# Kernel optimization log

Hardware: AMD Instinct MI355X
Metric: run time of the kernel (lower is better)

## Reference

```python
import jax, jax.numpy as jnp
import numpy as np

D_MODEL = 192
D_STATE = 16
D_CONV = 4
EXPAND = 2
D_INNER = EXPAND * D_MODEL          # 384
DT_RANK = (D_MODEL + 15) // 16       # 12
B_, C_, DD, HH, WW = 2, 192, 32, 32, 16


def setup_inputs() -> dict:
    key = jax.random.key(0)
    ks = jax.random.split(key, 10)
    s = 0.02
    return {
        "x": jax.random.normal(ks[0], (B_, C_, DD, HH, WW), jnp.float32),
        # Mamba params (mamba-ssm layout)
        "in_proj_w": jax.random.normal(ks[1], (2 * D_INNER, D_MODEL), jnp.float32) * s,
        "conv_w": jax.random.normal(ks[2], (D_INNER, 1, D_CONV), jnp.float32) * s,
        "conv_b": jnp.zeros((D_INNER,), jnp.float32),
        "x_proj_w": jax.random.normal(ks[3], (DT_RANK + 2 * D_STATE, D_INNER), jnp.float32) * s,
        "dt_proj_w": jax.random.normal(ks[4], (D_INNER, DT_RANK), jnp.float32) * s,
        # bias chosen so softplus(dt) is small/positive, as in mamba's dt init
        "dt_proj_b": jax.random.uniform(ks[5], (D_INNER,), jnp.float32, minval=-4.0, maxval=-2.0),
        "A_log": jnp.log(jnp.broadcast_to(jnp.arange(1, D_STATE + 1, dtype=jnp.float32), (D_INNER, D_STATE))),
        "D_param": jnp.ones((D_INNER,), jnp.float32),
        "out_proj_w": jax.random.normal(ks[6], (D_MODEL, D_INNER), jnp.float32) * s,
        # 1x1x1 Conv3d projection (input_dim -> output_dim)
        "proj_w": jax.random.normal(ks[7], (C_, C_), jnp.float32) * s,
        "proj_b": jnp.zeros((C_,), jnp.float32),
    }


def _mamba(xf, in_proj_w, conv_w, conv_b, x_proj_w, dt_proj_w, dt_proj_b, A_log, D_param, out_proj_w):
    # xf: (B, L, d_model)
    B, L, _ = xf.shape
    xz = xf @ in_proj_w.T                          # (B, L, 2*d_inner)
    u, z = jnp.split(xz, 2, axis=-1)               # each (B, L, d_inner)

    # causal depthwise conv1d over L, kernel D_CONV
    uc = jnp.transpose(u, (0, 2, 1))               # (B, d_inner, L)
    up = jnp.pad(uc, ((0, 0), (0, 0), (D_CONV - 1, 0)))
    conv = sum(up[:, :, k:k + L] * conv_w[None, :, 0, k, None] for k in range(D_CONV))
    conv = conv + conv_b[None, :, None]
    u = jax.nn.silu(jnp.transpose(conv, (0, 2, 1)))  # (B, L, d_inner)

    dbl = u @ x_proj_w.T                           # (B, L, dt_rank + 2*d_state)
    dt_low = dbl[..., :DT_RANK]
    Bm = dbl[..., DT_RANK:DT_RANK + D_STATE]       # (B, L, d_state)
    Cm = dbl[..., DT_RANK + D_STATE:]              # (B, L, d_state)
    dt = jax.nn.softplus(dt_low @ dt_proj_w.T + dt_proj_b)  # (B, L, d_inner)

    A = -jnp.exp(A_log)                            # (d_inner, d_state)

    def step(h, inputs):
        u_t, dt_t, B_t, C_t = inputs               # (B,d_inner),(B,d_inner),(B,d_state),(B,d_state)
        dA = jnp.exp(dt_t[..., None] * A)          # (B, d_inner, d_state)
        h = dA * h + dt_t[..., None] * B_t[:, None, :] * u_t[..., None]
        y = jnp.einsum('bds,bs->bd', h, C_t)
        return h, y

    h0 = jnp.zeros((B, D_INNER, D_STATE), xf.dtype)
    xs = (jnp.transpose(u, (1, 0, 2)), jnp.transpose(dt, (1, 0, 2)),
          jnp.transpose(Bm, (1, 0, 2)), jnp.transpose(Cm, (1, 0, 2)))
    _, ys = jax.lax.scan(step, h0, xs)             # ys: (L, B, d_inner)
    y = jnp.transpose(ys, (1, 0, 2)) + u * D_param
    y = y * jax.nn.silu(z)
    return y @ out_proj_w.T                        # (B, L, d_model)


def reference(x, in_proj_w, conv_w, conv_b, x_proj_w, dt_proj_w, dt_proj_b,
              A_log, D_param, out_proj_w, proj_w, proj_b):
    B, C, Dz, H, W = x.shape
    # InstanceNorm3d (affine=False, eps=1e-5, biased variance)
    mu = x.mean(axis=(2, 3, 4), keepdims=True)
    var = x.var(axis=(2, 3, 4), keepdims=True)
    xn = (x - mu) / jnp.sqrt(var + 1e-5)
    L = Dz * H * W
    xf = jnp.transpose(xn.reshape(B, C, L), (0, 2, 1))  # (B, L, C)
    y = _mamba(xf, in_proj_w, conv_w, conv_b, x_proj_w, dt_proj_w, dt_proj_b,
               A_log, D_param, out_proj_w)
    y = jnp.transpose(y, (0, 2, 1)).reshape(B, C, Dz, H, W)
    # 1x1x1 Conv3d projection
    out = jnp.einsum('bcdhw,oc->bodhw', y, proj_w) + proj_b[None, :, None, None, None]
    return out
```

## Files before the change

### kernel.cpp

```cpp
#include <hip/hip_runtime.h>
#include <hip/hip_bf16.h>
#include <hip/hip_fp16.h>
#include <math.h>

#define BB   2
#define CM   192
#define DI   384
#define LL   16384
#define NST  16
#define RDT  12
#define XJ   44
#define NC   512
#define CLEN 32
#define NCH  (NC / 16)
#define DBS  64
#define XZS  768
#define CVT  32
#define BK   32

typedef __attribute__((ext_vector_type(8))) short bf16x8;
typedef __attribute__((ext_vector_type(4))) float f32x4;
typedef __attribute__((ext_vector_type(2))) float f32x2;
typedef unsigned short ushort_t;

static __device__ __forceinline__ ushort_t f2bf(float f) {
  __hip_bfloat16 h = __float2bfloat16(f);
  return *reinterpret_cast<ushort_t*>(&h);
}
static __device__ __forceinline__ float bf2f(ushort_t u) {
  __hip_bfloat16 h;
  *reinterpret_cast<ushort_t*>(&h) = u;
  return __bfloat162float(h);
}
static __device__ __forceinline__ ushort_t f2h(float f) {
  __half h = __float2half(f);
  return *reinterpret_cast<ushort_t*>(&h);
}
static __device__ __forceinline__ float h2f(ushort_t u) {
  __half h;
  *reinterpret_cast<ushort_t*>(&h) = u;
  return __half2float(h);
}

__global__ __launch_bounds__(256) void fuse_proj_kernel(
    const float* __restrict__ pw, const float* __restrict__ ow, float* __restrict__ PW) {
  int idx = blockIdx.x * 256 + threadIdx.x;
  if (idx >= CM * DI) return;
  int o = idx / DI, d = idx % DI;
  float s = 0.f;
  #pragma unroll 4
  for (int c = 0; c < CM; c++) s += pw[o * CM + c] * ow[c * DI + d];
  PW[idx] = s;
}

__global__ __launch_bounds__(256) void cvt_weights_kernel(
    const float* __restrict__ ipw, const float* __restrict__ xpw,
    const float* __restrict__ PW,
    ushort_t* __restrict__ ipw_bf, ushort_t* __restrict__ xpw_bf,
    ushort_t* __restrict__ PW_bf) {
  int i = blockIdx.x * 256 + threadIdx.x;
  if (i < 2 * DI * CM) ipw_bf[i] = f2bf(ipw[i]);
  if (i < 128 * DI) {
    int r = i / DI;
    xpw_bf[i] = (r < XJ) ? f2bf(xpw[i]) : (ushort_t)0;
  }
  if (i < 256 * DI) {
    int r = i / DI;
    PW_bf[i] = (r < CM) ? f2bf(PW[i]) : (ushort_t)0;
  }
}

__global__ __launch_bounds__(256) void norm_stats_kernel(
    const float* __restrict__ x, float* __restrict__ mu, float* __restrict__ rstd) {
  int bc = blockIdx.x;
  const float* p = x + (size_t)bc * LL;
  float s = 0.f, ss = 0.f;
  for (int i = threadIdx.x * 4; i < LL; i += 256 * 4) {
    float4 v = *(const float4*)(p + i);
    s += v.x + v.y + v.z + v.w;
    ss += v.x * v.x + v.y * v.y + v.z * v.z + v.w * v.w;
  }
  for (int o = 32; o > 0; o >>= 1) {
    s += __shfl_down(s, o, 64);
    ss += __shfl_down(ss, o, 64);
  }
  __shared__ float sb[4], ssb[4];
  int wid = threadIdx.x >> 6;
  if ((threadIdx.x & 63) == 0) { sb[wid] = s; ssb[wid] = ss; }
  __syncthreads();
  if (threadIdx.x == 0) {
    s = sb[0] + sb[1] + sb[2] + sb[3];
    ss = ssb[0] + ssb[1] + ssb[2] + ssb[3];
    float m = s * (1.f / LL);
    float var = ss * (1.f / LL) - m * m;
    mu[bc] = m;
    rstd[bc] = 1.f / sqrtf(var + 1e-5f);
  }
}

__global__ __launch_bounds__(256) void xt_norm_kernel(
    const float* __restrict__ x, const float* __restrict__ mu,
    const float* __restrict__ rstd, ushort_t* __restrict__ xT) {
  __shared__ ushort_t T[64][72];
  int t0 = blockIdx.x * 64, c0 = blockIdx.y * 64, b = blockIdx.z;
  int tid = threadIdx.x;
  int c = tid >> 2, tq = (tid & 3) * 16;
  int bc = b * CM + c0 + c;
  const float* xp = x + (size_t)bc * LL + t0 + tq;
  float m = mu[bc], rs = rstd[bc];
  #pragma unroll
  for (int j = 0; j < 16; j += 4) {
    float4 v = *(const float4*)(xp + j);
    T[c][tq + j + 0] = f2bf((v.x - m) * rs);
    T[c][tq + j + 1] = f2bf((v.y - m) * rs);
    T[c][tq + j + 2] = f2bf((v.z - m) * rs);
    T[c][tq + j + 3] = f2bf((v.w - m) * rs);
  }
  __syncthreads();
  int t = tid >> 2, cq = (tid & 3) * 16;
  unsigned int ob[8];
  #pragma unroll
  for (int j = 0; j < 8; j++)
    ob[j] = (unsigned int)T[cq + 2 * j][t] | ((unsigned int)T[cq + 2 * j + 1][t] << 16);
  ushort_t* op = xT + ((size_t)b * LL + t0 + t) * CM + c0 + cq;
  *(uint4*)(op)     = make_uint4(ob[0], ob[1], ob[2], ob[3]);
  *(uint4*)(op + 8) = make_uint4(ob[4], ob[5], ob[6], ob[7]);
}

template <bool TOUT, typename OutT>
__global__ __launch_bounds__(256) void gemm_lds(
    const ushort_t* __restrict__ A, const ushort_t* __restrict__ BT,
    OutT* __restrict__ C, int K, int Mreal, int MT,
    long strideBT, long strideC, int ldc,
    const float* __restrict__ bias) {
  __shared__ ushort_t Asm[2][128 * BK];
  __shared__ ushort_t Bsm[2][128 * BK];

  int id = blockIdx.x;
  int per = MT * 8;
  int g = id / per, r = id % per;
  int nt = g * 8 + (r & 7);
  int mt = r >> 3;
  int b  = nt >> 7;
  long n0 = (long)(nt & 127) * 128;
  int m0 = mt * 128;

  int tid = threadIdx.x;
  int lane = tid & 63, wave = tid >> 6;
  const ushort_t* Bbase = BT + (size_t)b * strideBT;

  int srow0 = wave * 32 + (lane >> 2);
  int sk = (lane & 3) * 8;

  f32x4 acc[4][4];
  #pragma unroll
  for (int mi = 0; mi < 4; mi++)
    #pragma unroll
    for (int ni = 0; ni < 4; ni++) acc[mi][ni] = (f32x4){0.f, 0.f, 0.f, 0.f};

  int mh = wave & 1, nh = wave >> 1;
  int fr = lane & 15, fk = (lane >> 4) * 8;

  int nsteps = K / BK;
  {
    const ushort_t* As0 = A + (size_t)(m0 + srow0) * K + sk;
    const ushort_t* Bs0 = Bbase + (size_t)(n0 + srow0) * K + sk;
    __builtin_amdgcn_global_load_lds(As0, &Asm[0][wave * 1024], 16, 0, 0);
    __builtin_amdgcn_global_load_lds(As0 + (size_t)16 * K, &Asm[0][wave * 1024 + 512], 16, 0, 0);
    __builtin_amdgcn_global_load_lds(Bs0, &Bsm[0][wave * 1024], 16, 0, 0);
    __builtin_amdgcn_global_load_lds(Bs0 + (size_t)16 * K, &Bsm[0][wave * 1024 + 512], 16, 0, 0);
  }
  __syncthreads();
  int cur = 0;
  for (int s = 0; s < nsteps; s++) {
    if (s + 1 < nsteps) {
      int k0 = (s + 1) * BK;
      const ushort_t* As0 = A + (size_t)(m0 + srow0) * K + k0 + sk;
      const ushort_t* Bs0 = Bbase + (size_t)(n0 + srow0) * K + k0 + sk;
      __builtin_amdgcn_global_load_lds(As0, &Asm[cur ^ 1][wave * 1024], 16, 0, 0);
      __builtin_amdgcn_global_load_lds(As0 + (size_t)16 * K, &Asm[cur ^ 1][wave * 1024 + 512], 16, 0, 0);
      __builtin_amdgcn_global_load_lds(Bs0, &Bsm[cur ^ 1][wave * 1024], 16, 0, 0);
      __builtin_amdgcn_global_load_lds(Bs0 + (size_t)16 * K, &Bsm[cur ^ 1][wave * 1024 + 512], 16, 0, 0);
    }
    bf16x8 fa[4], fb[4];
    #pragma unroll
    for (int mi = 0; mi < 4; mi++)
      fa[mi] = *(const bf16x8*)&Asm[cur][(mh * 64 + mi * 16 + fr) * BK + fk];
    #pragma unroll
    for (int ni = 0; ni < 4; ni++)
      fb[ni] = *(const bf16x8*)&Bsm[cur][(nh * 64 + ni * 16 + fr) * BK + fk];
    #pragma unroll
    for (int mi = 0; mi < 4; mi++)
      #pragma unroll
      for (int ni = 0; ni < 4; ni++) {
        if constexpr (TOUT)
          acc[mi][ni] = __builtin_amdgcn_mfma_f32_16x16x32_bf16(fb[ni], fa[mi], acc[mi][ni], 0, 0, 0);
        else
          acc[mi][ni] = __builtin_amdgcn_mfma_f32_16x16x32_bf16(fa[mi], fb[ni], acc[mi][ni], 0, 0, 0);
      }
    __syncthreads();
    cur ^= 1;
  }

  int cq = (lane >> 4) * 4;
  if constexpr (TOUT) {
    #pragma unroll
    for (int ni = 0; ni < 4; ni++)
      #pragma unroll
      for (int rg = 0; rg < 4; rg++) {
        long n = n0 + nh * 64 + ni * 16 + cq + rg;
        OutT* cp = C + (size_t)b * strideC + n * ldc + m0 + mh * 64 + fr;
        #pragma unroll
        for (int mi = 0; mi < 4; mi++) {
          int mrow = m0 + mh * 64 + mi * 16 + fr;
          if (mrow < Mreal) {
            float v = acc[mi][ni][rg];
            if constexpr (sizeof(OutT) == 2) cp[mi * 16] = f2bf(v);
            else                             cp[mi * 16] = v;
          }
        }
      }
  } else {
    #pragma unroll
    for (int mi = 0; mi < 4; mi++)
      #pragma unroll
      for (int rg = 0; rg < 4; rg++) {
        int m = m0 + mh * 64 + mi * 16 + cq + rg;
        if (m < Mreal) {
          float bv = bias ? bias[m] : 0.f;
          OutT* cp = C + (size_t)b * strideC + (size_t)m * ldc + n0 + nh * 64 + fr;
          #pragma unroll
          for (int ni = 0; ni < 4; ni++)
            cp[ni * 16] = acc[mi][ni][rg] + bv;
        }
      }
  }
}

__global__ __launch_bounds__(384) void conv_silu_kernel(
    const ushort_t* __restrict__ xzT, const float* __restrict__ conv_w,
    const float* __restrict__ conv_b, ushort_t* __restrict__ u_t) {
  __shared__ ushort_t Us[CVT + 3][DI];
  int t0 = blockIdx.x * CVT;
  int b = blockIdx.y;
  int tid = threadIdx.x;
  #pragma unroll
  for (int r = 0; r < CVT + 3; r++) {
    int t = t0 - 3 + r;
    Us[r][tid] = (t >= 0) ? xzT[((size_t)b * LL + t) * XZS + tid] : (ushort_t)0;
  }
  float w0 = conv_w[tid * 4 + 0], w1 = conv_w[tid * 4 + 1];
  float w2 = conv_w[tid * 4 + 2], w3 = conv_w[tid * 4 + 3];
  float cb = conv_b[tid];
  __syncthreads();
  ushort_t* up = u_t + ((size_t)b * LL + t0) * DI + tid;
  float xm3 = bf2f(Us[0][tid]);
  float xm2 = bf2f(Us[1][tid]);
  float xm1 = bf2f(Us[2][tid]);
  #pragma unroll
  for (int t = 0; t < CVT; t++) {
    float xc = bf2f(Us[t + 3][tid]);
    float a = cb + w3 * xc + w2 * xm1 + w1 * xm2 + w0 * xm3;
    float sv = a / (1.f + __expf(-a));
    up[(size_t)t * DI] = f2bf(sv);
    xm3 = xm2; xm2 = xm1; xm1 = xc;
  }
}

__global__ __launch_bounds__(128) void scan_phase1(
    const ushort_t* __restrict__ u_t, const float* __restrict__ dblT,
    const float* __restrict__ A_log,
    const float* __restrict__ dtw, const float* __restrict__ dtb,
    float* __restrict__ hend, float* __restrict__ Sbuf,
    ushort_t* __restrict__ dt16) {
  int chunk = blockIdx.x, b = blockIdx.z;
  int d = blockIdx.y * 128 + threadIdx.x;
  int t0 = chunk * CLEN;
  const float* dblB = dblT + ((size_t)b * LL + t0) * DBS;
  int bd = b * DI + d;
  float av0 = -expf(A_log[d * NST]);
  float av_[NST];
  bool ok = true;
  #pragma unroll
  for (int j = 0; j < NST; j++) {
    av_[j] = -expf(A_log[d * NST + j]);
    ok = ok && (fabsf(av_[j] - av0 * (float)(j + 1)) <= 1e-4f * fabsf(av_[j]));
  }
  float w12[12];
  #pragma unroll
  for (int rr = 0; rr < 12; rr += 4)
    *(float4*)(w12 + rr) = *(const float4*)(dtw + d * 12 + rr);
  float db = dtb[d];
  const ushort_t* up = u_t + ((size_t)b * LL + t0) * DI + d;
  ushort_t* dtp16 = dt16 + ((size_t)b * LL + t0) * DI + d;
  float S = 0.f;

  size_t o = ((size_t)bd * NC + chunk) * NST;
  if (__all(ok)) {
    f32x2 h2[8];
    #pragma unroll
    for (int j = 0; j < 8; j++) h2[j] = (f32x2){0.f, 0.f};
    #pragma unroll 4
    for (int t = 0; t < CLEN; t++) {
      float4 L0 = *(const float4*)(dblB + t * DBS + 0);
      float4 L1 = *(const float4*)(dblB + t * DBS + 4);
      float4 L2 = *(const float4*)(dblB + t * DBS + 8);
      float4 B0 = *(const float4*)(dblB + t * DBS + RDT + 0);
      float4 B1 = *(const float4*)(dblB + t * DBS + RDT + 4);
      float4 B2 = *(const float4*)(dblB + t * DBS + RDT + 8);
      float4 B3 = *(const float4*)(dblB + t * DBS + RDT + 12);
      float acc = db;
      acc = fmaf(L0.x, w12[0], acc); acc = fmaf(L0.y, w12[1], acc);
      acc = fmaf(L0.z, w12[2], acc); acc = fmaf(L0.w, w12[3], acc);
      acc = fmaf(L1.x, w12[4], acc); acc = fmaf(L1.y, w12[5], acc);
      acc = fmaf(L1.z, w12[6], acc); acc = fmaf(L1.w, w12[7], acc);
      acc = fmaf(L2.x, w12[8], acc); acc = fmaf(L2.y, w12[9], acc);
      acc = fmaf(L2.z, w12[10], acc); acc = fmaf(L2.w, w12[11], acc);
      float dtv = (acc > 15.f) ? acc : __logf(1.f + __expf(acc));
      dtp16[(size_t)t * DI] = f2h(dtv);
      float uv  = bf2f(up[(size_t)t * DI]);
      float q = dtv * uv;
      S += dtv;
      float p1 = __expf(dtv * av0);
      float p2 = p1 * p1, p4 = p2 * p2, p8 = p4 * p4;
      f32x2 p2v = {p2, p2}, p4v = {p4, p4}, p8v = {p8, p8};
      f32x2 P0 = {p1, p2};
      f32x2 P1 = P0 * p2v;
      f32x2 P2 = P0 * p4v;
      f32x2 P3 = P1 * p4v;
      f32x2 P4 = P0 * p8v;
      f32x2 P5 = P1 * p8v;
      f32x2 P6 = P2 * p8v;
      f32x2 P7 = P3 * p8v;
      f32x2 qv = {q, q};
      h2[0] = P0 * h2[0] + qv * (f32x2){B0.x, B0.y};
      h2[1] = P1 * h2[1] + qv * (f32x2){B0.z, B0.w};
      h2[2] = P2 * h2[2] + qv * (f32x2){B1.x, B1.y};
      h2[3] = P3 * h2[3] + qv * (f32x2){B1.z, B1.w};
      h2[4] = P4 * h2[4] + qv * (f32x2){B2.x, B2.y};
      h2[5] = P5 * h2[5] + qv * (f32x2){B2.z, B2.w};
      h2[6] = P6 * h2[6] + qv * (f32x2){B3.x, B3.y};
      h2[7] = P7 * h2[7] + qv * (f32x2){B3.z, B3.w};
    }
    #pragma unroll
    for (int j = 0; j < 8; j += 2)
      *(float4*)(hend + o + j * 2) =
          make_float4(h2[j].x, h2[j].y, h2[j + 1].x, h2[j + 1].y);
  } else {
    float h[NST];
    #pragma unroll
    for (int j = 0; j < NST; j++) h[j] = 0.f;
    for (int t = 0; t < CLEN; t++) {
      float acc = db;
      #pragma unroll
      for (int rr = 0; rr < 12; rr++) acc = fmaf(dblB[t * DBS + rr], w12[rr], acc);
      float dtv = (acc > 15.f) ? acc : __logf(1.f + __expf(acc));
      dtp16[(size_t)t * DI] = f2h(dtv);
      float uv  = bf2f(up[(size_t)t * DI]);
      float q = dtv * uv;
      S += dtv;
      #pragma unroll
      for (int j = 0; j < NST; j++)
        h[j] = __expf(dtv * av_[j]) * h[j] + q * dblB[t * DBS + RDT + j];
    }
    #pragma unroll
    for (int j = 0; j < NST; j++) hend[o + j] = h[j];
  }
  Sbuf[(size_t)bd * NC + chunk] = S;
}

__global__ __launch_bounds__(256) void scan_combine(
    float* __restrict__ hend, const float* __restrict__ Sbuf,
    const float* __restrict__ A_log) {
  __shared__ float sP[16][16], sH[16][16];
  int bd = blockIdx.x;
  int d = bd % DI;
  int s = threadIdx.x & 15, g = threadIdx.x >> 4;
  float av = -expf(A_log[d * NST + s]);
  size_t baseS = (size_t)bd * NC + g * NCH;
  size_t base = ((size_t)bd * NC + g * NCH) * NST + s;
  float Pl = 1.f, Hl = 0.f;
  #pragma unroll
  for (int k = 0; k < NCH; k++) {
    float p = __expf(Sbuf[baseS + k] * av);
    Hl = fmaf(p, Hl, hend[base + (size_t)k * NST]);
    Pl *= p;
  }
  sP[g][s] = Pl; sH[g][s] = Hl;
  __syncthreads();
  if (threadIdx.x < 16) {
    int ss = threadIdx.x;
    float c = 0.f;
    #pragma unroll
    for (int gg = 0; gg < 16; gg++) {
      float tmp = sH[gg][ss];
      float pp  = sP[gg][ss];
      sH[gg][ss] = c;
      c = fmaf(pp, c, tmp);
    }
  }
  __syncthreads();
  float c = sH[g][s];
  #pragma unroll
  for (int k = 0; k < NCH; k++) {
    size_t o = base + (size_t)k * NST;
    float p = __expf(Sbuf[baseS + k] * av);
    float he = hend[o];
    hend[o] = c;
    c = fmaf(p, c, he);
  }
}

__global__ __launch_bounds__(128) void scan_phase3(
    const ushort_t* __restrict__ u_t, const float* __restrict__ dblT,
    const float* __restrict__ A_log, const ushort_t* __restrict__ dt16,
    const float* __restrict__ hin, const float* __restrict__ Dp,
    const ushort_t* __restrict__ xzT, ushort_t* __restrict__ ym_t) {
  int chunk = blockIdx.x, b = blockIdx.z;
  int d = blockIdx.y * 128 + threadIdx.x;
  int t0 = chunk * CLEN;
  const float* dblB = dblT + ((size_t)b * LL + t0) * DBS;
  int bd = b * DI + d;
  float av0 = -expf(A_log[d * NST]);
  float av_[NST];
  bool ok = true;
  #pragma unroll
  for (int j = 0; j < NST; j++) {
    av_[j] = -expf(A_log[d * NST + j]);
    ok = ok && (fabsf(av_[j] - av0 * (float)(j + 1)) <= 1e-4f * fabsf(av_[j]));
  }
  const ushort_t* up = u_t + ((size_t)b * LL + t0) * DI + d;
  const ushort_t* zp = xzT + ((size_t)b * LL + t0) * XZS + DI + d;
  const ushort_t* dtp16 = dt16 + ((size_t)b * LL + t0) * DI + d;
  ushort_t* ymp = ym_t + ((size_t)b * LL + t0) * DI + d;

  const float* hi = hin + ((size_t)bd * NC + chunk) * NST;
  float Dv = Dp[d];

  if (__all(ok)) {
    f32x2 h2[8];
    #pragma unroll
    for (int j = 0; j < 8; j += 2) {
      float4 v = *(const float4*)(hi + j * 2);
      h2[j]     = (f32x2){v.x, v.y};
      h2[j + 1] = (f32x2){v.z, v.w};
    }
    #pragma unroll 4
    for (int t = 0; t < CLEN; t++) {
      float4 B0 = *(const float4*)(dblB + t * DBS + RDT + 0);
      float4 B1 = *(const float4*)(dblB + t * DBS + RDT + 4);
      float4 B2 = *(const float4*)(dblB + t * DBS + RDT + 8);
      float4 B3 = *(const float4*)(dblB + t * DBS + RDT + 12);
      float4 C0 = *(const float4*)(dblB + t * DBS + RDT + 16);
      float4 C1 = *(const float4*)(dblB + t * DBS + RDT + 20);
      float4 C2 = *(const float4*)(dblB + t * DBS + RDT + 24);
      float4 C3 = *(const float4*)(dblB + t * DBS + RDT + 28);
      float dtv = h2f(dtp16[(size_t)t * DI]);
      float uv  = bf2f(up[(size_t)t * DI]);
      float zv  = bf2f(zp[(size_t)t * XZS]);
      float q = dtv * uv;
      float p1 = __expf(dtv * av0);
      float p2 = p1 * p1, p4 = p2 * p2, p8 = p4 * p4;
      f32x2 p2v = {p2, p2}, p4v = {p4, p4}, p8v = {p8, p8};
      f32x2 P0 = {p1, p2};
      f32x2 P1 = P0 * p2v;
      f32x2 P2 = P0 * p4v;
      f32x2 P3 = P1 * p4v;
      f32x2 P4 = P0 * p8v;
      f32x2 P5 = P1 * p8v;
      f32x2 P6 = P2 * p8v;
      f32x2 P7 = P3 * p8v;
      f32x2 qv = {q, q};
      f32x2 ya, yb;
      h2[0] = P0 * h2[0] + qv * (f32x2){B0.x, B0.y};  ya = h2[0] * (f32x2){C0.x, C0.y};
      h2[1] = P1 * h2[1] + qv * (f32x2){B0.z, B0.w};  yb = h2[1] * (f32x2){C0.z, C0.w};
      h2[2] = P2 * h2[2] + qv * (f32x2){B1.x, B1.y};  ya = h2[2] * (f32x2){C1.x, C1.y} + ya;
      h2[3] = P3 * h2[3] + qv * (f32x2){B1.z, B1.w};  yb = h2[3] * (f32x2){C1.z, C1.w} + yb;
      h2[4] = P4 * h2[4] + qv * (f32x2){B2.x, B2.y};  ya = h2[4] * (f32x2){C2.x, C2.y} + ya;
      h2[5] = P5 * h2[5] + qv * (f32x2){B2.z, B2.w};  yb = h2[5] * (f32x2){C2.z, C2.w} + yb;
      h2[6] = P6 * h2[6] + qv * (f32x2){B3.x, B3.y};  ya = h2[6] * (f32x2){C3.x, C3.y} + ya;
      h2[7] = P7 * h2[7] + qv * (f32x2){B3.z, B3.w};  yb = h2[7] * (f32x2){C3.z, C3.w} + yb;
      float y = (ya.x + ya.y) + (yb.x + yb.y);
      float yv = (y + uv * Dv) * (zv / (1.f + __expf(-zv)));
      ymp[(size_t)t * DI] = f2bf(yv);
    }
  } else {
    float h[NST];
    #pragma unroll
    for (int j = 0; j < NST; j++) h[j] = hi[j];
    for (int t = 0; t < CLEN; t++) {
      float dtv = h2f(dtp16[(size_t)t * DI]);
      float uv  = bf2f(up[(size_t)t * DI]);
      float zv  = bf2f(zp[(size_t)t * XZS]);
      float q = dtv * uv;
      float y = 0.f;
      #pragma unroll
      for (int j = 0; j < NST; j++) {
        h[j] = __expf(dtv * av_[j]) * h[j] + q * dblB[t * DBS + RDT + j];
        y = fmaf(h[j], dblB[t * DBS + RDT + NST + j], y);
      }
      float yv = (y + uv * Dv) * (zv / (1.f + __expf(-zv)));
      ymp[(size_t)t * DI] = f2bf(yv);
    }
  }
}

extern "C" void kernel_launch(void* const* d_in, const int* in_sizes, int n_in,
                              void* d_out, int out_size, void* d_ws, size_t ws_size,
                              hipStream_t stream) {
  const float* x         = (const float*)d_in[0];
  const float* in_proj_w = (const float*)d_in[1];
  const float* conv_w    = (const float*)d_in[2];
  const float* conv_b    = (const float*)d_in[3];
  const float* x_proj_w  = (const float*)d_in[4];
  const float* dt_proj_w = (const float*)d_in[5];
  const float* dt_proj_b = (const float*)d_in[6];
  const float* A_log     = (const float*)d_in[7];
  const float* D_param   = (const float*)d_in[8];
  const float* out_proj_w= (const float*)d_in[9];
  const float* proj_w    = (const float*)d_in[10];
  const float* proj_b    = (const float*)d_in[11];
  float* out = (float*)d_out;

  float* w = (float*)d_ws;
  float*    mu     = w;
  float*    rstd   = w + 512;
  float*    PW     = w + 1024;
  ushort_t* PW_bf  = (ushort_t*)(w + 74752);
  ushort_t* ipw_bf = (ushort_t*)(w + 123904);
  ushort_t* xpw_bf = (ushort_t*)(w + 197632);
  ushort_t* xT     = (ushort_t*)(w + 222208);
  ushort_t* xzT    = (ushort_t*)(w + 3367936);
  ushort_t* u_t    = (ushort_t*)(w + 15950848);
  float*    dblT   = w + 22242304;
  ushort_t* ym_t   = (ushort_t*)(w + 24339456);
  float*    hend   = w + 30630912;
  float*    Sbuf   = w + 36922368;
  ushort_t* dt16   = (ushort_t*)(w + 37315584);
  size_t need = 43607040;
  if (ws_size < need * sizeof(float)) return;

  norm_stats_kernel<<<dim3(BB * CM), dim3(256), 0, stream>>>(x, mu, rstd);
  fuse_proj_kernel<<<dim3((CM * DI + 255) / 256), dim3(256), 0, stream>>>(proj_w, out_proj_w, PW);
  cvt_weights_kernel<<<dim3((2 * DI * CM + 255) / 256), dim3(256), 0, stream>>>(
      in_proj_w, x_proj_w, PW, ipw_bf, xpw_bf, PW_bf);
  xt_norm_kernel<<<dim3(LL / 64, CM / 64, BB), dim3(256), 0, stream>>>(x, mu, rstd, xT);

  gemm_lds<true, ushort_t><<<dim3(256 * 6), dim3(256), 0, stream>>>(
      ipw_bf, xT, xzT, CM, 768, 6, (long)LL * CM, (long)LL * XZS, XZS, nullptr);

  conv_silu_kernel<<<dim3(LL / CVT, BB), dim3(384), 0, stream>>>(xzT, conv_w, conv_b, u_t);

  gemm_lds<true, float><<<dim3(256 * 1), dim3(256), 0, stream>>>(
      xpw_bf, u_t, dblT, DI, 64, 1, (long)LL * DI, (long)LL * DBS, DBS, nullptr);

  scan_phase1<<<dim3(NC, 3, BB), dim3(128), 0, stream>>>(
      u_t, dblT, A_log, dt_proj_w, dt_proj_b, hend, Sbuf, dt16);
  scan_combine<<<dim3(BB * DI), dim3(256), 0, stream>>>(hend, Sbuf, A_log);
  scan_phase3<<<dim3(NC, 3, BB), dim3(128), 0, stream>>>(
      u_t, dblT, A_log, dt16, hend, D_param, xzT, ym_t);

  gemm_lds<false, float><<<dim3(256 * 2), dim3(256), 0, stream>>>(
      PW_bf, ym_t, out, DI, CM, 2, (long)LL * DI, (long)CM * LL, LL, proj_b);
}
```

Measured before the change: 189.1 us.

## Stage per-chunk dbl rows in shared memory and double the scan chunk length

Phase-1 and phase-3 scan kernels now cooperatively load each chunk's dt/B/C rows into LDS once per block, then read them as broadcast LDS loads instead of per-thread global loads. The chunk length is doubled to 64 (256 chunks), which halves the combine work and hend/Sbuf traffic but also halves the number of blocks in the scan phases, reducing available parallelism. A __syncthreads and extra LDS usage are added per block.

```diff
diff --git a/kernel.cpp b/kernel.cpp
--- a/kernel.cpp
+++ b/kernel.cpp
@@ -10,8 +10,8 @@
 #define NST  16
 #define RDT  12
 #define XJ   44
-#define NC   512
-#define CLEN 32
+#define NC   256
+#define CLEN 64
 #define NCH  (NC / 16)
 #define DBS  64
 #define XZS  768
@@ -273,10 +273,15 @@
     const float* __restrict__ dtw, const float* __restrict__ dtb,
     float* __restrict__ hend, float* __restrict__ Sbuf,
     ushort_t* __restrict__ dt16) {
+  __shared__ __align__(16) float Ds[CLEN][48];
   int chunk = blockIdx.x, b = blockIdx.z;
   int d = blockIdx.y * 128 + threadIdx.x;
   int t0 = chunk * CLEN;
   const float* dblB = dblT + ((size_t)b * LL + t0) * DBS;
+  for (int i = threadIdx.x; i < CLEN * 11; i += 128) {
+    int row = i / 11, c4 = (i % 11) * 4;
+    *(float4*)(&Ds[row][c4]) = *(const float4*)(dblB + row * DBS + c4);
+  }
   int bd = b * DI + d;
   float av0 = -expf(A_log[d * NST]);
   float av_[NST];
@@ -294,21 +299,22 @@
   const ushort_t* up = u_t + ((size_t)b * LL + t0) * DI + d;
   ushort_t* dtp16 = dt16 + ((size_t)b * LL + t0) * DI + d;
   float S = 0.f;
+  __syncthreads();
 
   size_t o = ((size_t)bd * NC + chunk) * NST;
   if (__all(ok)) {
     f32x2 h2[8];
     #pragma unroll
     for (int j = 0; j < 8; j++) h2[j] = (f32x2){0.f, 0.f};
-    #pragma unroll 4
+    #pragma unroll 2
     for (int t = 0; t < CLEN; t++) {
-      float4 L0 = *(const float4*)(dblB + t * DBS + 0);
-      float4 L1 = *(const float4*)(dblB + t * DBS + 4);
-      float4 L2 = *(const float4*)(dblB + t * DBS + 8);
-      float4 B0 = *(const float4*)(dblB + t * DBS + RDT + 0);
-      float4 B1 = *(const float4*)(dblB + t * DBS + RDT + 4);
-      float4 B2 = *(const float4*)(dblB + t * DBS + RDT + 8);
-      float4 B3 = *(const float4*)(dblB + t * DBS + RDT + 12);
+      float4 L0 = *(const float4*)(&Ds[t][0]);
+      float4 L1 = *(const float4*)(&Ds[t][4]);
+      float4 L2 = *(const float4*)(&Ds[t][8]);
+      float4 B0 = *(const float4*)(&Ds[t][12]);
+      float4 B1 = *(const float4*)(&Ds[t][16]);
+      float4 B2 = *(const float4*)(&Ds[t][20]);
+      float4 B3 = *(const float4*)(&Ds[t][24]);
       float acc = db;
       acc = fmaf(L0.x, w12[0], acc); acc = fmaf(L0.y, w12[1], acc);
       acc = fmaf(L0.z, w12[2], acc); acc = fmaf(L0.w, w12[3], acc);
@@ -353,7 +359,7 @@
     for (int t = 0; t < CLEN; t++) {
       float acc = db;
       #pragma unroll
-      for (int rr = 0; rr < 12; rr++) acc = fmaf(dblB[t * DBS + rr], w12[rr], acc);
+      for (int rr = 0; rr < 12; rr++) acc = fmaf(Ds[t][rr], w12[rr], acc);
       float dtv = (acc > 15.f) ? acc : __logf(1.f + __expf(acc));
       dtp16[(size_t)t * DI] = f2h(dtv);
       float uv  = bf2f(up[(size_t)t * DI]);
@@ -361,7 +367,7 @@
       S += dtv;
       #pragma unroll
       for (int j = 0; j < NST; j++)
-        h[j] = __expf(dtv * av_[j]) * h[j] + q * dblB[t * DBS + RDT + j];
+        h[j] = __expf(dtv * av_[j]) * h[j] + q * Ds[t][12 + j];
     }
     #pragma unroll
     for (int j = 0; j < NST; j++) hend[o + j] = h[j];
@@ -416,10 +422,15 @@
     const float* __restrict__ A_log, const ushort_t* __restrict__ dt16,
     const float* __restrict__ hin, const float* __restrict__ Dp,
     const ushort_t* __restrict__ xzT, ushort_t* __restrict__ ym_t) {
+  __shared__ __align__(16) float Ds[CLEN][32];
   int chunk = blockIdx.x, b = blockIdx.z;
   int d = blockIdx.y * 128 + threadIdx.x;
   int t0 = chunk * CLEN;
   const float* dblB = dblT + ((size_t)b * LL + t0) * DBS;
+  for (int i = threadIdx.x; i < CLEN * 8; i += 128) {
+    int row = i >> 3, c4 = (i & 7) * 4;
+    *(float4*)(&Ds[row][c4]) = *(const float4*)(dblB + row * DBS + RDT + c4);
+  }
   int bd = b * DI + d;
   float av0 = -expf(A_log[d * NST]);
   float av_[NST];
@@ -436,6 +447,7 @@
 
   const float* hi = hin + ((size_t)bd * NC + chunk) * NST;
   float Dv = Dp[d];
+  __syncthreads();
 
   if (__all(ok)) {
     f32x2 h2[8];
@@ -445,16 +457,16 @@
       h2[j]     = (f32x2){v.x, v.y};
       h2[j + 1] = (f32x2){v.z, v.w};
     }
-    #pragma unroll 4
+    #pragma unroll 2
     for (int t = 0; t < CLEN; t++) {
-      float4 B0 = *(const float4*)(dblB + t * DBS + RDT + 0);
-      float4 B1 = *(const float4*)(dblB + t * DBS + RDT + 4);
-      float4 B2 = *(const float4*)(dblB + t * DBS + RDT + 8);
-      float4 B3 = *(const float4*)(dblB + t * DBS + RDT + 12);
-      float4 C0 = *(const float4*)(dblB + t * DBS + RDT + 16);
-      float4 C1 = *(const float4*)(dblB + t * DBS + RDT + 20);
-      float4 C2 = *(const float4*)(dblB + t * DBS + RDT + 24);
-      float4 C3 = *(const float4*)(dblB + t * DBS + RDT + 28);
+      float4 B0 = *(const float4*)(&Ds[t][0]);
+      float4 B1 = *(const float4*)(&Ds[t][4]);
+      float4 B2 = *(const float4*)(&Ds[t][8]);
+      float4 B3 = *(const float4*)(&Ds[t][12]);
+      float4 C0 = *(const float4*)(&Ds[t][16]);
+      float4 C1 = *(const float4*)(&Ds[t][20]);
+      float4 C2 = *(const float4*)(&Ds[t][24]);
+      float4 C3 = *(const float4*)(&Ds[t][28]);
       float dtv = h2f(dtp16[(size_t)t * DI]);
       float uv  = bf2f(up[(size_t)t * DI]);
       float zv  = bf2f(zp[(size_t)t * XZS]);
@@ -496,8 +508,8 @@
       float y = 0.f;
       #pragma unroll
       for (int j = 0; j < NST; j++) {
-        h[j] = __expf(dtv * av_[j]) * h[j] + q * dblB[t * DBS + RDT + j];
-        y = fmaf(h[j], dblB[t * DBS + RDT + NST + j], y);
+        h[j] = __expf(dtv * av_[j]) * h[j] + q * Ds[t][j];
+        y = fmaf(h[j], Ds[t][16 + j], y);
       }
       float yv = (y + uv * Dv) * (zv / (1.f + __expf(-zv)));
       ymp[(size_t)t * DI] = f2bf(yv);
```

Measured after the change: 201.7 us. 1.07x slower.

## Store u and dt in channel-major layout for vectorized scan loads

Applied to the files above, without the earlier changes.

The conv kernel now also writes a second copy of u in a (b, d, t) layout, packing 8 bf16 timesteps per thread into 16-byte stores. The scan phase1 and phase3 kernels read u and write or read dt16 as uint4 vectors along time instead of strided 2-byte accesses. The goal is to cut the number of memory transactions in the scan kernels. In exchange, the conv kernel writes extra bytes, its per-thread stores in the new layout are strided across lanes by LL, and the workspace grows.

```diff
diff --git a/kernel.cpp b/kernel.cpp
--- a/kernel.cpp
+++ b/kernel.cpp
@@ -239,7 +239,8 @@
 
 __global__ __launch_bounds__(384) void conv_silu_kernel(
     const ushort_t* __restrict__ xzT, const float* __restrict__ conv_w,
-    const float* __restrict__ conv_b, ushort_t* __restrict__ u_t) {
+    const float* __restrict__ conv_b, ushort_t* __restrict__ u_t,
+    ushort_t* __restrict__ u_s) {
   __shared__ ushort_t Us[CVT + 3][DI];
   int t0 = blockIdx.x * CVT;
   int b = blockIdx.y;
@@ -254,6 +255,7 @@
   float cb = conv_b[tid];
   __syncthreads();
   ushort_t* up = u_t + ((size_t)b * LL + t0) * DI + tid;
+  unsigned pk[CVT / 2];
   float xm3 = bf2f(Us[0][tid]);
   float xm2 = bf2f(Us[1][tid]);
   float xm1 = bf2f(Us[2][tid]);
@@ -262,13 +264,20 @@
     float xc = bf2f(Us[t + 3][tid]);
     float a = cb + w3 * xc + w2 * xm1 + w1 * xm2 + w0 * xm3;
     float sv = a / (1.f + __expf(-a));
-    up[(size_t)t * DI] = f2bf(sv);
+    ushort_t sb = f2bf(sv);
+    up[(size_t)t * DI] = sb;
+    if (t & 1) pk[t >> 1] |= ((unsigned)sb) << 16;
+    else       pk[t >> 1] = (unsigned)sb;
     xm3 = xm2; xm2 = xm1; xm1 = xc;
   }
+  ushort_t* usp = u_s + ((size_t)b * DI + tid) * LL + t0;
+  #pragma unroll
+  for (int g = 0; g < CVT / 8; g++)
+    *(uint4*)(usp + g * 8) = make_uint4(pk[g*4], pk[g*4+1], pk[g*4+2], pk[g*4+3]);
 }
 
 __global__ __launch_bounds__(128) void scan_phase1(
-    const ushort_t* __restrict__ u_t, const float* __restrict__ dblT,
+    const ushort_t* __restrict__ u_s, const float* __restrict__ dblT,
     const float* __restrict__ A_log,
     const float* __restrict__ dtw, const float* __restrict__ dtb,
     float* __restrict__ hend, float* __restrict__ Sbuf,
@@ -291,8 +300,8 @@
   for (int rr = 0; rr < 12; rr += 4)
     *(float4*)(w12 + rr) = *(const float4*)(dtw + d * 12 + rr);
   float db = dtb[d];
-  const ushort_t* up = u_t + ((size_t)b * LL + t0) * DI + d;
-  ushort_t* dtp16 = dt16 + ((size_t)b * LL + t0) * DI + d;
+  const ushort_t* ubp = u_s + (size_t)bd * LL + t0;
+  ushort_t* dtp = dt16 + (size_t)bd * LL + t0;
   float S = 0.f;
 
   size_t o = ((size_t)bd * NC + chunk) * NST;
@@ -300,47 +309,57 @@
     f32x2 h2[8];
     #pragma unroll
     for (int j = 0; j < 8; j++) h2[j] = (f32x2){0.f, 0.f};
-    #pragma unroll 4
-    for (int t = 0; t < CLEN; t++) {
-      float4 L0 = *(const float4*)(dblB + t * DBS + 0);
-      float4 L1 = *(const float4*)(dblB + t * DBS + 4);
-      float4 L2 = *(const float4*)(dblB + t * DBS + 8);
-      float4 B0 = *(const float4*)(dblB + t * DBS + RDT + 0);
-      float4 B1 = *(const float4*)(dblB + t * DBS + RDT + 4);
-      float4 B2 = *(const float4*)(dblB + t * DBS + RDT + 8);
-      float4 B3 = *(const float4*)(dblB + t * DBS + RDT + 12);
-      float acc = db;
-      acc = fmaf(L0.x, w12[0], acc); acc = fmaf(L0.y, w12[1], acc);
-      acc = fmaf(L0.z, w12[2], acc); acc = fmaf(L0.w, w12[3], acc);
-      acc = fmaf(L1.x, w12[4], acc); acc = fmaf(L1.y, w12[5], acc);
-      acc = fmaf(L1.z, w12[6], acc); acc = fmaf(L1.w, w12[7], acc);
-      acc = fmaf(L2.x, w12[8], acc); acc = fmaf(L2.y, w12[9], acc);
-      acc = fmaf(L2.z, w12[10], acc); acc = fmaf(L2.w, w12[11], acc);
-      float dtv = (acc > 15.f) ? acc : __logf(1.f + __expf(acc));
-      dtp16[(size_t)t * DI] = f2h(dtv);
-      float uv  = bf2f(up[(size_t)t * DI]);
-      float q = dtv * uv;
-      S += dtv;
-      float p1 = __expf(dtv * av0);
-      float p2 = p1 * p1, p4 = p2 * p2, p8 = p4 * p4;
-      f32x2 p2v = {p2, p2}, p4v = {p4, p4}, p8v = {p8, p8};
-      f32x2 P0 = {p1, p2};
-      f32x2 P1 = P0 * p2v;
-      f32x2 P2 = P0 * p4v;
-      f32x2 P3 = P1 * p4v;
-      f32x2 P4 = P0 * p8v;
-      f32x2 P5 = P1 * p8v;
-      f32x2 P6 = P2 * p8v;
-      f32x2 P7 = P3 * p8v;
-      f32x2 qv = {q, q};
-      h2[0] = P0 * h2[0] + qv * (f32x2){B0.x, B0.y};
-      h2[1] = P1 * h2[1] + qv * (f32x2){B0.z, B0.w};
-      h2[2] = P2 * h2[2] + qv * (f32x2){B1.x, B1.y};
-      h2[3] = P3 * h2[3] + qv * (f32x2){B1.z, B1.w};
-      h2[4] = P4 * h2[4] + qv * (f32x2){B2.x, B2.y};
-      h2[5] = P5 * h2[5] + qv * (f32x2){B2.z, B2.w};
-      h2[6] = P6 * h2[6] + qv * (f32x2){B3.x, B3.y};
-      h2[7] = P7 * h2[7] + qv * (f32x2){B3.z, B3.w};
+    #pragma unroll
+    for (int tg = 0; tg < CLEN; tg += 8) {
+      uint4 uq = *(const uint4*)(ubp + tg);
+      const unsigned* uw = (const unsigned*)&uq;
+      unsigned dqw[4];
+      #pragma unroll
+      for (int k = 0; k < 8; k++) {
+        int t = tg + k;
+        float4 L0 = *(const float4*)(dblB + t * DBS + 0);
+        float4 L1 = *(const float4*)(dblB + t * DBS + 4);
+        float4 L2 = *(const float4*)(dblB + t * DBS + 8);
+        float4 B0 = *(const float4*)(dblB + t * DBS + RDT + 0);
+        float4 B1 = *(const float4*)(dblB + t * DBS + RDT + 4);
+        float4 B2 = *(const float4*)(dblB + t * DBS + RDT + 8);
+        float4 B3 = *(const float4*)(dblB + t * DBS + RDT + 12);
+        float acc = db;
+        acc = fmaf(L0.x, w12[0], acc); acc = fmaf(L0.y, w12[1], acc);
+        acc = fmaf(L0.z, w12[2], acc); acc = fmaf(L0.w, w12[3], acc);
+        acc = fmaf(L1.x, w12[4], acc); acc = fmaf(L1.y, w12[5], acc);
+        acc = fmaf(L1.z, w12[6], acc); acc = fmaf(L1.w, w12[7], acc);
+        acc = fmaf(L2.x, w12[8], acc); acc = fmaf(L2.y, w12[9], acc);
+        acc = fmaf(L2.z, w12[10], acc); acc = fmaf(L2.w, w12[11], acc);
+        float dtv = (acc > 15.f) ? acc : __logf(1.f + __expf(acc));
+        unsigned dh = (unsigned)f2h(dtv);
+        if (k & 1) dqw[k >> 1] |= dh << 16;
+        else       dqw[k >> 1] = dh;
+        float uv = bf2f((ushort_t)(uw[k >> 1] >> ((k & 1) * 16)));
+        float q = dtv * uv;
+        S += dtv;
+        float p1 = __expf(dtv * av0);
+        float p2 = p1 * p1, p4 = p2 * p2, p8 = p4 * p4;
+        f32x2 p2v = {p2, p2}, p4v = {p4, p4}, p8v = {p8, p8};
+        f32x2 P0 = {p1, p2};
+        f32x2 P1 = P0 * p2v;
+        f32x2 P2 = P0 * p4v;
+        f32x2 P3 = P1 * p4v;
+        f32x2 P4 = P0 * p8v;
+        f32x2 P5 = P1 * p8v;
+        f32x2 P6 = P2 * p8v;
+        f32x2 P7 = P3 * p8v;
+        f32x2 qv = {q, q};
+        h2[0] = P0 * h2[0] + qv * (f32x2){B0.x, B0.y};
+        h2[1] = P1 * h2[1] + qv * (f32x2){B0.z, B0.w};
+        h2[2] = P2 * h2[2] + qv * (f32x2){B1.x, B1.y};
+        h2[3] = P3 * h2[3] + qv * (f32x2){B1.z, B1.w};
+        h2[4] = P4 * h2[4] + qv * (f32x2){B2.x, B2.y};
+        h2[5] = P5 * h2[5] + qv * (f32x2){B2.z, B2.w};
+        h2[6] = P6 * h2[6] + qv * (f32x2){B3.x, B3.y};
+        h2[7] = P7 * h2[7] + qv * (f32x2){B3.z, B3.w};
+      }
+      *(uint4*)(dtp + tg) = make_uint4(dqw[0], dqw[1], dqw[2], dqw[3]);
     }
     #pragma unroll
     for (int j = 0; j < 8; j += 2)
@@ -355,8 +374,8 @@
       #pragma unroll
       for (int rr = 0; rr < 12; rr++) acc = fmaf(dblB[t * DBS + rr], w12[rr], acc);
       float dtv = (acc > 15.f) ? acc : __logf(1.f + __expf(acc));
-      dtp16[(size_t)t * DI] = f2h(dtv);
-      float uv  = bf2f(up[(size_t)t * DI]);
+      dtp[t] = f2h(dtv);
+      float uv  = bf2f(ubp[t]);
       float q = dtv * uv;
       S += dtv;
       #pragma unroll
@@ -412,7 +431,7 @@
 }
 
 __global__ __launch_bounds__(128) void scan_phase3(
-    const ushort_t* __restrict__ u_t, const float* __restrict__ dblT,
+    const ushort_t* __restrict__ u_s, const float* __restrict__ dblT,
     const float* __restrict__ A_log, const ushort_t* __restrict__ dt16,
     const float* __restrict__ hin, const float* __restrict__ Dp,
     const ushort_t* __restrict__ xzT, ushort_t* __restrict__ ym_t) {
@@ -429,9 +448,9 @@
     av_[j] = -expf(A_log[d * NST + j]);
     ok = ok && (fabsf(av_[j] - av0 * (float)(j + 1)) <= 1e-4f * fabsf(av_[j]));
   }
-  const ushort_t* up = u_t + ((size_t)b * LL + t0) * DI + d;
+  const ushort_t* ubp = u_s + (size_t)bd * LL + t0;
+  const ushort_t* dtp = dt16 + (size_t)bd * LL + t0;
   const ushort_t* zp = xzT + ((size_t)b * LL + t0) * XZS + DI + d;
-  const ushort_t* dtp16 = dt16 + ((size_t)b * LL + t0) * DI + d;
   ushort_t* ymp = ym_t + ((size_t)b * LL + t0) * DI + d;
 
   const float* hi = hin + ((size_t)bd * NC + chunk) * NST;
@@ -445,52 +464,60 @@
       h2[j]     = (f32x2){v.x, v.y};
       h2[j + 1] = (f32x2){v.z, v.w};
     }
-    #pragma unroll 4
-    for (int t = 0; t < CLEN; t++) {
-      float4 B0 = *(const float4*)(dblB + t * DBS + RDT + 0);
-      float4 B1 = *(const float4*)(dblB + t * DBS + RDT + 4);
-      float4 B2 = *(const float4*)(dblB + t * DBS + RDT + 8);
-      float4 B3 = *(const float4*)(dblB + t * DBS + RDT + 12);
-      float4 C0 = *(const float4*)(dblB + t * DBS + RDT + 16);
-      float4 C1 = *(const float4*)(dblB + t * DBS + RDT + 20);
-      float4 C2 = *(const float4*)(dblB + t * DBS + RDT + 24);
-      float4 C3 = *(const float4*)(dblB + t * DBS + RDT + 28);
-      float dtv = h2f(dtp16[(size_t)t * DI]);
-      float uv  = bf2f(up[(size_t)t * DI]);
-      float zv  = bf2f(zp[(size_t)t * XZS]);
-      float q = dtv * uv;
-      float p1 = __expf(dtv * av0);
-      float p2 = p1 * p1, p4 = p2 * p2, p8 = p4 * p4;
-      f32x2 p2v = {p2, p2}, p4v = {p4, p4}, p8v = {p8, p8};
-      f32x2 P0 = {p1, p2};
-      f32x2 P1 = P0 * p2v;
-      f32x2 P2 = P0 * p4v;
-      f32x2 P3 = P1 * p4v;
-      f32x2 P4 = P0 * p8v;
-      f32x2 P5 = P1 * p8v;
-      f32x2 P6 = P2 * p8v;
-      f32x2 P7 = P3 * p8v;
-      f32x2 qv = {q, q};
-      f32x2 ya, yb;
-      h2[0] = P0 * h2[0] + qv * (f32x2){B0.x, B0.y};  ya = h2[0] * (f32x2){C0.x, C0.y};
-      h2[1] = P1 * h2[1] + qv * (f32x2){B0.z, B0.w};  yb = h2[1] * (f32x2){C0.z, C0.w};
-      h2[2] = P2 * h2[2] + qv * (f32x2){B1.x, B1.y};  ya = h2[2] * (f32x2){C1.x, C1.y} + ya;
-      h2[3] = P3 * h2[3] + qv * (f32x2){B1.z, B1.w};  yb = h2[3] * (f32x2){C1.z, C1.w} + yb;
-      h2[4] = P4 * h2[4] + qv * (f32x2){B2.x, B2.y};  ya = h2[4] * (f32x2){C2.x, C2.y} + ya;
-      h2[5] = P5 * h2[5] + qv * (f32x2){B2.z, B2.w};  yb = h2[5] * (f32x2){C2.z, C2.w} + yb;
-      h2[6] = P6 * h2[6] + qv * (f32x2){B3.x, B3.y};  ya = h2[6] * (f32x2){C3.x, C3.y} + ya;
-      h2[7] = P7 * h2[7] + qv * (f32x2){B3.z, B3.w};  yb = h2[7] * (f32x2){C3.z, C3.w} + yb;
-      float y = (ya.x + ya.y) + (yb.x + yb.y);
-      float yv = (y + uv * Dv) * (zv / (1.f + __expf(-zv)));
-      ymp[(size_t)t * DI] = f2bf(yv);
+    #pragma unroll
+    for (int tg = 0; tg < CLEN; tg += 8) {
+      uint4 uq = *(const uint4*)(ubp + tg);
+      uint4 dq = *(const uint4*)(dtp + tg);
+      const unsigned* uw = (const unsigned*)&uq;
+      const unsigned* dw = (const unsigned*)&dq;
+      #pragma unroll
+      for (int k = 0; k < 8; k++) {
+        int t = tg + k;
+        float4 B0 = *(const float4*)(dblB + t * DBS + RDT + 0);
+        float4 B1 = *(const float4*)(dblB + t * DBS + RDT + 4);
+        float4 B2 = *(const float4*)(dblB + t * DBS + RDT + 8);
+        float4 B3 = *(const float4*)(dblB + t * DBS + RDT + 12);
+        float4 C0 = *(const float4*)(dblB + t * DBS + RDT + 16);
+        float4 C1 = *(const float4*)(dblB + t * DBS + RDT + 20);
+        float4 C2 = *(const float4*)(dblB + t * DBS + RDT + 24);
+        float4 C3 = *(const float4*)(dblB + t * DBS + RDT + 28);
+        float dtv = h2f((ushort_t)(dw[k >> 1] >> ((k & 1) * 16)));
+        float uv  = bf2f((ushort_t)(uw[k >> 1] >> ((k & 1) * 16)));
+        float zv  = bf2f(zp[(size_t)t * XZS]);
+        float q = dtv * uv;
+        float p1 = __expf(dtv * av0);
+        float p2 = p1 * p1, p4 = p2 * p2, p8 = p4 * p4;
+        f32x2 p2v = {p2, p2}, p4v = {p4, p4}, p8v = {p8, p8};
+        f32x2 P0 = {p1, p2};
+        f32x2 P1 = P0 * p2v;
+        f32x2 P2 = P0 * p4v;
+        f32x2 P3 = P1 * p4v;
+        f32x2 P4 = P0 * p8v;
+        f32x2 P5 = P1 * p8v;
+        f32x2 P6 = P2 * p8v;
+        f32x2 P7 = P3 * p8v;
+        f32x2 qv = {q, q};
+        f32x2 ya, yb;
+        h2[0] = P0 * h2[0] + qv * (f32x2){B0.x, B0.y};  ya = h2[0] * (f32x2){C0.x, C0.y};
+        h2[1] = P1 * h2[1] + qv * (f32x2){B0.z, B0.w};  yb = h2[1] * (f32x2){C0.z, C0.w};
+        h2[2] = P2 * h2[2] + qv * (f32x2){B1.x, B1.y};  ya = h2[2] * (f32x2){C1.x, C1.y} + ya;
+        h2[3] = P3 * h2[3] + qv * (f32x2){B1.z, B1.w};  yb = h2[3] * (f32x2){C1.z, C1.w} + yb;
+        h2[4] = P4 * h2[4] + qv * (f32x2){B2.x, B2.y};  ya = h2[4] * (f32x2){C2.x, C2.y} + ya;
+        h2[5] = P5 * h2[5] + qv * (f32x2){B2.z, B2.w};  yb = h2[5] * (f32x2){C2.z, C2.w} + yb;
+        h2[6] = P6 * h2[6] + qv * (f32x2){B3.x, B3.y};  ya = h2[6] * (f32x2){C3.x, C3.y} + ya;
+        h2[7] = P7 * h2[7] + qv * (f32x2){B3.z, B3.w};  yb = h2[7] * (f32x2){C3.z, C3.w} + yb;
+        float y = (ya.x + ya.y) + (yb.x + yb.y);
+        float yv = (y + uv * Dv) * (zv / (1.f + __expf(-zv)));
+        ymp[(size_t)t * DI] = f2bf(yv);
+      }
     }
   } else {
     float h[NST];
     #pragma unroll
     for (int j = 0; j < NST; j++) h[j] = hi[j];
     for (int t = 0; t < CLEN; t++) {
-      float dtv = h2f(dtp16[(size_t)t * DI]);
-      float uv  = bf2f(up[(size_t)t * DI]);
+      float dtv = h2f(dtp[t]);
+      float uv  = bf2f(ubp[t]);
       float zv  = bf2f(zp[(size_t)t * XZS]);
       float q = dtv * uv;
       float y = 0.f;
@@ -537,7 +564,8 @@
   float*    hend   = w + 30630912;
   float*    Sbuf   = w + 36922368;
   ushort_t* dt16   = (ushort_t*)(w + 37315584);
-  size_t need = 43607040;
+  ushort_t* u_s    = (ushort_t*)(w + 43607040);
+  size_t need = 49898496;
   if (ws_size < need * sizeof(float)) return;
 
   norm_stats_kernel<<<dim3(BB * CM), dim3(256), 0, stream>>>(x, mu, rstd);
@@ -549,16 +577,16 @@
   gemm_lds<true, ushort_t><<<dim3(256 * 6), dim3(256), 0, stream>>>(
       ipw_bf, xT, xzT, CM, 768, 6, (long)LL * CM, (long)LL * XZS, XZS, nullptr);
 
-  conv_silu_kernel<<<dim3(LL / CVT, BB), dim3(384), 0, stream>>>(xzT, conv_w, conv_b, u_t);
+  conv_silu_kernel<<<dim3(LL / CVT, BB), dim3(384), 0, stream>>>(xzT, conv_w, conv_b, u_t, u_s);
 
   gemm_lds<true, float><<<dim3(256 * 1), dim3(256), 0, stream>>>(
       xpw_bf, u_t, dblT, DI, 64, 1, (long)LL * DI, (long)LL * DBS, DBS, nullptr);
 
   scan_phase1<<<dim3(NC, 3, BB), dim3(128), 0, stream>>>(
-      u_t, dblT, A_log, dt_proj_w, dt_proj_b, hend, Sbuf, dt16);
+      u_s, dblT, A_log, dt_proj_w, dt_proj_b, hend, Sbuf, dt16);
   scan_combine<<<dim3(BB * DI), dim3(256), 0, stream>>>(hend, Sbuf, A_log);
   scan_phase3<<<dim3(NC, 3, BB), dim3(128), 0, stream>>>(
-      u_t, dblT, A_log, dt16, hend, D_param, xzT, ym_t);
+      u_s, dblT, A_log, dt16, hend, D_param, xzT, ym_t);
 
   gemm_lds<false, float><<<dim3(256 * 2), dim3(256), 0, stream>>>(
       PW_bf, ym_t, out, DI, CM, 2, (long)LL * DI, (long)CM * LL, LL, proj_b);
```

New measurement: 231.1 us, median of 4. 1.22x slower.
